# Kernel optimization log

Hardware: AMD Instinct MI355X
Metric: run time of the kernel (lower is better)

The kernel has to match this reference:

```python
import jax, jax.numpy as jnp
import numpy as np

D = 512; H = 8; DH = D // H; DFF = 4 * D; INNER = 2 * D; K = 31
B = 8; S = 1024
EPS = 1e-5


def layer_norm(x, g, b):
    m = jnp.mean(x, axis=-1, keepdims=True)
    v = jnp.mean(jnp.square(x - m), axis=-1, keepdims=True)
    return (x - m) * jax.lax.rsqrt(v + EPS) * g + b


def setup_inputs() -> dict:
    key = jax.random.key(0)
    ks = iter(jax.random.split(key, 32))
    w = lambda *s: jax.random.normal(next(ks), s, dtype=jnp.float32) * 0.02
    d = {
        "x": jax.random.normal(next(ks), (B, S, D), dtype=jnp.float32),
        # FF module 1
        "ln1_g": jnp.ones((D,)), "ln1_b": jnp.zeros((D,)),
        "ff1_w1": w(DFF, D), "ff1_b1": jnp.zeros((DFF,)),
        "ff1_w2": w(D, DFF), "ff1_b2": jnp.zeros((D,)),
        # attention
        "lna_g": jnp.ones((D,)), "lna_b": jnp.zeros((D,)),
        "qkv_w": w(3 * D, D), "qkv_b": jnp.zeros((3 * D,)),
        "out_w": w(D, D), "out_b": jnp.zeros((D,)),
        # conv module
        "lnc_g": jnp.ones((D,)), "lnc_b": jnp.zeros((D,)),
        "pw1_w": w(INNER, D), "pw1_b": jnp.zeros((INNER,)),
        "dw_w": w(D, 1, K), "dw_b": jnp.zeros((D,)),
        "bn_g": jnp.ones((D,)), "bn_b": jnp.zeros((D,)),
        "bn_mean": jnp.zeros((D,)), "bn_var": jnp.ones((D,)),
        "pw2_w": w(D, D), "pw2_b": jnp.zeros((D,)),
        # FF module 2
        "ln2_g": jnp.ones((D,)), "ln2_b": jnp.zeros((D,)),
        "ff2_w1": w(DFF, D), "ff2_b1": jnp.zeros((DFF,)),
        "ff2_w2": w(D, DFF), "ff2_b2": jnp.zeros((D,)),
        # final layer norm
        "lnf_g": jnp.ones((D,)), "lnf_b": jnp.zeros((D,)),
    }
    return d


def _ff(x, g, b, w1, b1, w2, b2):
    h = layer_norm(x, g, b)
    h = jax.nn.silu(h @ w1.T + b1)
    h = h @ w2.T + b2
    return h + x  # FeedForwardModule adds its own residual


def _attn(x, g, b, qkv_w, qkv_b, out_w, out_b):
    h = layer_norm(x, g, b)
    qkv = (h @ qkv_w.T + qkv_b).reshape(B, S, 3, H, DH)
    q, k, v = qkv[:, :, 0], qkv[:, :, 1], qkv[:, :, 2]  # [B,S,H,DH]
    scores = jnp.einsum('bqhd,bkhd->bhqk', q, k) / np.sqrt(DH).astype(np.float32)
    probs = jax.nn.softmax(scores, axis=-1)
    ctx = jnp.einsum('bhqk,bkhd->bqhd', probs, v).reshape(B, S, D)
    return ctx @ out_w.T + out_b


def _conv(x, g, b, pw1_w, pw1_b, dw_w, dw_b, bn_g, bn_b, bn_mean, bn_var, pw2_w, pw2_b):
    h = layer_norm(x, g, b)
    y = h @ pw1_w.T + pw1_b                      # [B,S,2D] pointwise conv1
    a, gate = jnp.split(y, 2, axis=-1)           # GLU along channel dim
    y = a * jax.nn.sigmoid(gate)                 # [B,S,D]
    y = y.transpose(0, 2, 1)                     # [B,D,S]
    y = jax.lax.conv_general_dilated(
        y, dw_w, window_strides=(1,), padding=((K // 2, K // 2),),
        dimension_numbers=('NCH', 'OIH', 'NCH'), feature_group_count=D)
    y = y + dw_b[None, :, None]
    y = (y - bn_mean[None, :, None]) * jax.lax.rsqrt(bn_var + EPS)[None, :, None]
    y = y * bn_g[None, :, None] + bn_b[None, :, None]
    y = jax.nn.silu(y)
    y = y.transpose(0, 2, 1)                     # [B,S,D]
    y = y @ pw2_w.T + pw2_b
    return y + x  # ConvModule adds its own residual


def reference(x, ln1_g, ln1_b, ff1_w1, ff1_b1, ff1_w2, ff1_b2,
              lna_g, lna_b, qkv_w, qkv_b, out_w, out_b,
              lnc_g, lnc_b, pw1_w, pw1_b, dw_w, dw_b,
              bn_g, bn_b, bn_mean, bn_var, pw2_w, pw2_b,
              ln2_g, ln2_b, ff2_w1, ff2_b1, ff2_w2, ff2_b2,
              lnf_g, lnf_b):
    x = x + 0.5 * _ff(x, ln1_g, ln1_b, ff1_w1, ff1_b1, ff1_w2, ff1_b2)
    x = x + _attn(x, lna_g, lna_b, qkv_w, qkv_b, out_w, out_b)
    x = x + _conv(x, lnc_g, lnc_b, pw1_w, pw1_b, dw_w, dw_b,
                  bn_g, bn_b, bn_mean, bn_var, pw2_w, pw2_b)
    x = x + 0.5 * _ff(x, ln2_g, ln2_b, ff2_w1, ff2_b1, ff2_w2, ff2_b2)
    return layer_norm(x, lnf_g, lnf_b)
```

## Files before the change

### kernel.cpp

```cpp
#include <hip/hip_runtime.h>
#include <hip/hip_bf16.h>

typedef __attribute__((ext_vector_type(8))) short bf16x8;
typedef __attribute__((ext_vector_type(4))) short bf16x4;
typedef __attribute__((ext_vector_type(4))) float f32x4;

#define NTOK 8192
#define SEQ  1024
#define NH   8

__device__ __forceinline__ float bfs2f(short s) {
  union { unsigned u; float f; } x; x.u = ((unsigned)(unsigned short)s) << 16; return x.f;
}
__device__ __forceinline__ short f2bfs(float f) {
  __hip_bfloat16 h = __float2bfloat16(f);
  return *reinterpret_cast<short*>(&h);
}
__device__ __forceinline__ float bfp2f(const __hip_bfloat16* p) {
  return bfs2f(*reinterpret_cast<const short*>(p));
}

__device__ __forceinline__ void gld16(const void* g, void* l) {
  __builtin_amdgcn_global_load_lds(
      (__attribute__((address_space(1))) void*)const_cast<void*>(g),
      (__attribute__((address_space(3))) void*)l, 16, 0, 0);
}

struct WSeg { const float* src; unsigned dst_off; unsigned nvec; };
struct WPack { WSeg s[8]; };

__global__ __launch_bounds__(256) void cast_wall_kernel(WPack p,
                                                        __hip_bfloat16* __restrict__ dst) {
  unsigned v = blockIdx.x * 256 + threadIdx.x;
#pragma unroll
  for (int t = 0; t < 8; ++t) {
    if (v < p.s[t].nvec) {
      const float* s = p.s[t].src + (size_t)v * 8;
      f32x4 a = *reinterpret_cast<const f32x4*>(s);
      f32x4 b = *reinterpret_cast<const f32x4*>(s + 4);
      bf16x8 o;
#pragma unroll
      for (int j = 0; j < 4; ++j) { o[j] = f2bfs(a[j]); o[4 + j] = f2bfs(b[j]); }
      *reinterpret_cast<bf16x8*>(reinterpret_cast<short*>(dst) +
                                 (size_t)(p.s[t].dst_off + v) * 8) = o;
      return;
    }
    v -= p.s[t].nvec;
  }
}

__global__ __launch_bounds__(256) void cast_dww_kernel(const float* __restrict__ src,
                                                       __hip_bfloat16* __restrict__ dst) {
  for (int k = 0; k < 31; ++k)
    for (int c = threadIdx.x; c < 512; c += 256)
      dst[k * 512 + c] = __float2bfloat16(src[c * 31 + k]);
}

struct PtrPack { const void* p[23]; };

__global__ __launch_bounds__(256) void cast_small_kernel(PtrPack pk,
                                                         __hip_bfloat16* __restrict__ dst) {
  constexpr int sizes[23] = {512, 512, 2048, 512, 512, 512, 1536, 512, 512, 512, 1024, 512,
                             512, 512, 512, 512, 512, 512, 512, 2048, 512, 512, 512};
  int off = 0;
  for (int t = 0; t < 23; ++t) {
    const int n = sizes[t];
    for (int i = threadIdx.x; i < n; i += 256)
      dst[off + i] = __float2bfloat16(((const float*)pk.p[t])[i]);
    off += n;
  }
}

__global__ void ws_bad_kernel(float* __restrict__ out) {
  if (threadIdx.x == 0) out[0] = 5000.f;
}

__global__ __launch_bounds__(256) void lnb_kernel(const __hip_bfloat16* __restrict__ in,
                                                  const __hip_bfloat16* __restrict__ g,
                                                  const __hip_bfloat16* __restrict__ b,
                                                  __hip_bfloat16* __restrict__ out) {
  const int wv = threadIdx.x >> 6, ln = threadIdx.x & 63;
  const int row = blockIdx.x * 4 + wv;
  bf16x8 iv = *reinterpret_cast<const bf16x8*>(in + (size_t)row * 512 + ln * 8);
  float v[8];
#pragma unroll
  for (int j = 0; j < 8; ++j) v[j] = bfs2f(iv[j]);
  float s = 0.f;
#pragma unroll
  for (int j = 0; j < 8; ++j) s += v[j];
  for (int m = 1; m < 64; m <<= 1) s += __shfl_xor(s, m);
  const float mean = s * (1.f / 512.f);
  float q = 0.f;
#pragma unroll
  for (int j = 0; j < 8; ++j) { float d = v[j] - mean; q += d * d; }
  for (int m = 1; m < 64; m <<= 1) q += __shfl_xor(q, m);
  const float rstd = rsqrtf(q * (1.f / 512.f) + 1e-5f);
  bf16x8 gg = *reinterpret_cast<const bf16x8*>(g + ln * 8);
  bf16x8 bb = *reinterpret_cast<const bf16x8*>(b + ln * 8);
  bf16x8 ov;
#pragma unroll
  for (int j = 0; j < 8; ++j)
    ov[j] = f2bfs((v[j] - mean) * rstd * bfs2f(gg[j]) + bfs2f(bb[j]));
  *reinterpret_cast<bf16x8*>(out + (size_t)row * 512 + ln * 8) = ov;
}

__global__ __launch_bounds__(256) void ln_kernel(const float* __restrict__ in,
                                                 const __hip_bfloat16* __restrict__ g,
                                                 const __hip_bfloat16* __restrict__ b,
                                                 __hip_bfloat16* __restrict__ out) {
  const int wv = threadIdx.x >> 6, ln = threadIdx.x & 63;
  const int row = blockIdx.x * 4 + wv;
  const float* p = in + (size_t)row * 512 + ln * 8;
  float v[8];
  {
    const f32x4* p4 = reinterpret_cast<const f32x4*>(p);
    f32x4 a = p4[0], c = p4[1];
#pragma unroll
    for (int j = 0; j < 4; ++j) { v[j] = a[j]; v[4 + j] = c[j]; }
  }
  float s = 0.f;
#pragma unroll
  for (int j = 0; j < 8; ++j) s += v[j];
  for (int m = 1; m < 64; m <<= 1) s += __shfl_xor(s, m);
  const float mean = s * (1.f / 512.f);
  float q = 0.f;
#pragma unroll
  for (int j = 0; j < 8; ++j) { float d = v[j] - mean; q += d * d; }
  for (int m = 1; m < 64; m <<= 1) q += __shfl_xor(q, m);
  const float rstd = rsqrtf(q * (1.f / 512.f) + 1e-5f);
  bf16x8 gg = *reinterpret_cast<const bf16x8*>(g + ln * 8);
  bf16x8 bb = *reinterpret_cast<const bf16x8*>(b + ln * 8);
  bf16x8 ov;
#pragma unroll
  for (int j = 0; j < 8; ++j)
    ov[j] = f2bfs((v[j] - mean) * rstd * bfs2f(gg[j]) + bfs2f(bb[j]));
  *reinterpret_cast<bf16x8*>(out + (size_t)row * 512 + ln * 8) = ov;
}

__global__ __launch_bounds__(256) void lnf_kernel(const __hip_bfloat16* __restrict__ in,
                                                  const __hip_bfloat16* __restrict__ g,
                                                  const __hip_bfloat16* __restrict__ b,
                                                  float* __restrict__ out) {
  const int wv = threadIdx.x >> 6, ln = threadIdx.x & 63;
  const int row = blockIdx.x * 4 + wv;
  bf16x8 iv = *reinterpret_cast<const bf16x8*>(in + (size_t)row * 512 + ln * 8);
  float v[8];
#pragma unroll
  for (int j = 0; j < 8; ++j) v[j] = bfs2f(iv[j]);
  float s = 0.f;
#pragma unroll
  for (int j = 0; j < 8; ++j) s += v[j];
  for (int m = 1; m < 64; m <<= 1) s += __shfl_xor(s, m);
  const float mean = s * (1.f / 512.f);
  float q = 0.f;
#pragma unroll
  for (int j = 0; j < 8; ++j) { float d = v[j] - mean; q += d * d; }
  for (int m = 1; m < 64; m <<= 1) q += __shfl_xor(q, m);
  const float rstd = rsqrtf(q * (1.f / 512.f) + 1e-5f);
  bf16x8 gg = *reinterpret_cast<const bf16x8*>(g + ln * 8);
  bf16x8 bb = *reinterpret_cast<const bf16x8*>(b + ln * 8);
  f32x4 o0, o1;
#pragma unroll
  for (int j = 0; j < 4; ++j) {
    o0[j] = (v[j] - mean) * rstd * bfs2f(gg[j]) + bfs2f(bb[j]);
    o1[j] = (v[4 + j] - mean) * rstd * bfs2f(gg[4 + j]) + bfs2f(bb[4 + j]);
  }
  float* op = out + (size_t)row * 512 + ln * 8;
  *reinterpret_cast<f32x4*>(op) = o0;
  *reinterpret_cast<f32x4*>(op + 4) = o1;
}

template <int EPI>
__global__ __launch_bounds__(256, 3) void gemm_bt(const __hip_bfloat16* __restrict__ A,
                                                  const __hip_bfloat16* __restrict__ W,
                                                  const __hip_bfloat16* __restrict__ bias,
                                                  __hip_bfloat16* __restrict__ outb,
                                                  __hip_bfloat16* __restrict__ vTout,
                                                  int K, int M) {
  __shared__ __align__(16) __hip_bfloat16 As[128 * 64];
  __shared__ __align__(16) __hip_bfloat16 Bs[128 * 64];
  const int tid = threadIdx.x;
  const int wv = tid >> 6, ln = tid & 63;
  const int hi = ln >> 4, lo = ln & 15;
  const int lo7 = lo & 7;
  const int gx = gridDim.x;
  const int nwg = gx * gridDim.y;
  const int t = blockIdx.y * gx + blockIdx.x;
  const int w = (t & 7) * (nwg >> 3) + (t >> 3);
  const int n0 = (w & (gx - 1)) * 128;
  const int m0 = (w / gx) * 128;
  const int wr = wv >> 1, wc = wv & 1;
  const int srow = ln >> 3;
  const int scolz = (((ln & 7) ^ srow) << 3);

  f32x4 acc[4][4] = {};

  for (int k0 = 0; k0 < K; k0 += 64) {
    __syncthreads();
#pragma unroll
    for (int i = 0; i < 4; ++i) {
      const int grp = i * 4 + wv;
      const int row = grp * 8 + srow;
      gld16(A + (size_t)(n0 + row) * K + k0 + scolz, As + grp * 512);
      gld16(W + (size_t)(m0 + row) * K + k0 + scolz, Bs + grp * 512);
    }
    __syncthreads();
#pragma unroll
    for (int kk2 = 0; kk2 < 2; ++kk2) {
      const int g0 = ((kk2 * 4 + hi) ^ lo7) << 3;
      bf16x8 af[4], bfr[4];
#pragma unroll
      for (int r = 0; r < 4; ++r)
        af[r] = *reinterpret_cast<const bf16x8*>(As + (wr * 64 + r * 16 + lo) * 64 + g0);
#pragma unroll
      for (int c = 0; c < 4; ++c)
        bfr[c] = *reinterpret_cast<const bf16x8*>(Bs + (wc * 64 + c * 16 + lo) * 64 + g0);
#pragma unroll
      for (int r = 0; r < 4; ++r)
#pragma unroll
        for (int c = 0; c < 4; ++c)
          acc[r][c] = __builtin_amdgcn_mfma_f32_16x16x32_bf16(af[r], bfr[c], acc[r][c], 0, 0, 0);
    }
  }

#pragma unroll
  for (int r = 0; r < 4; ++r) {
#pragma unroll
    for (int c = 0; c < 4; ++c) {
      const int m = m0 + wc * 64 + c * 16 + lo;
      const float bv = bfp2f(bias + m);
      const int nb = n0 + wr * 64 + r * 16 + hi * 4;
      if constexpr (EPI == 3) {
        if (m >= 1024) {
          const int hd = m - 1024;
          __hip_bfloat16* vp = vTout +
              ((size_t)((nb >> 10) * NH + (hd >> 6)) * 64 + (hd & 63)) * 1024 + (nb & 1023);
          bf16x4 vv;
#pragma unroll
          for (int j = 0; j < 4; ++j) vv[j] = f2bfs(acc[r][c][j] + bv);
          *reinterpret_cast<bf16x4*>(vp) = vv;
          continue;
        }
      }
#pragma unroll
      for (int j = 0; j < 4; ++j) {
        const int n = nb + j;
        float v = acc[r][c][j] + bv;
        if constexpr (EPI == 1) v = v / (1.f + __expf(-v));
        outb[(size_t)n * M + m] = __float2bfloat16(v);
      }
    }
  }
}

template <int RF32>
__global__ __launch_bounds__(256, 4) void gemm64_resid(const __hip_bfloat16* __restrict__ A,
                                                       const __hip_bfloat16* __restrict__ W,
                                                       const __hip_bfloat16* __restrict__ bias,
                                                       const void* __restrict__ rsrc,
                                                       __hip_bfloat16* __restrict__ resid,
                                                       int K, float alpha, float beta) {
  __shared__ __align__(16) __hip_bfloat16 As[64 * 64];
  __shared__ __align__(16) __hip_bfloat16 Bs[128 * 64];
  const int tid = threadIdx.x;
  const int wv = tid >> 6, ln = tid & 63;
  const int hi = ln >> 4, lo = ln & 15;
  const int lo7 = lo & 7;
  const int gx = gridDim.x;
  const int nwg = gx * gridDim.y;
  const int t = blockIdx.y * gx + blockIdx.x;
  const int w = (t & 7) * (nwg >> 3) + (t >> 3);
  const int n0 = (w & (gx - 1)) * 64;
  const int m0 = (w / gx) * 128;
  const int wr = wv >> 1, wc = wv & 1;
  const int srow = ln >> 3;
  const int scolz = (((ln & 7) ^ srow) << 3);

  f32x4 acc[2][4] = {};

  for (int k0 = 0; k0 < K; k0 += 64) {
    __syncthreads();
#pragma unroll
    for (int i = 0; i < 2; ++i) {
      const int grp = i * 4 + wv;
      gld16(A + (size_t)(n0 + grp * 8 + srow) * K + k0 + scolz, As + grp * 512);
    }
#pragma unroll
    for (int i = 0; i < 4; ++i) {
      const int grp = i * 4 + wv;
      gld16(W + (size_t)(m0 + grp * 8 + srow) * K + k0 + scolz, Bs + grp * 512);
    }
    __syncthreads();
#pragma unroll
    for (int kk2 = 0; kk2 < 2; ++kk2) {
      const int g0 = ((kk2 * 4 + hi) ^ lo7) << 3;
      bf16x8 af[2], bfr[4];
#pragma unroll
      for (int r = 0; r < 2; ++r)
        af[r] = *reinterpret_cast<const bf16x8*>(As + (wr * 32 + r * 16 + lo) * 64 + g0);
#pragma unroll
      for (int c = 0; c < 4; ++c)
        bfr[c] = *reinterpret_cast<const bf16x8*>(Bs + (wc * 64 + c * 16 + lo) * 64 + g0);
#pragma unroll
      for (int r = 0; r < 2; ++r)
#pragma unroll
        for (int c = 0; c < 4; ++c)
          acc[r][c] = __builtin_amdgcn_mfma_f32_16x16x32_bf16(af[r], bfr[c], acc[r][c], 0, 0, 0);
    }
  }

#pragma unroll
  for (int r = 0; r < 2; ++r) {
#pragma unroll
    for (int c = 0; c < 4; ++c) {
      const int m = m0 + wc * 64 + c * 16 + lo;
      const float bv = bfp2f(bias + m);
#pragma unroll
      for (int j = 0; j < 4; ++j) {
        const int n = n0 + wr * 32 + r * 16 + hi * 4 + j;
        const size_t idx = (size_t)n * 512 + m;
        const float rv = RF32 ? ((const float*)rsrc)[idx]
                              : bfs2f(((const short*)rsrc)[idx]);
        resid[idx] = __float2bfloat16(alpha * rv + beta * (acc[r][c][j] + bv));
      }
    }
  }
}

__global__ __launch_bounds__(256, 3) void gemm_glu(const __hip_bfloat16* __restrict__ A,
                                                   const __hip_bfloat16* __restrict__ W,
                                                   const __hip_bfloat16* __restrict__ bias,
                                                   __hip_bfloat16* __restrict__ outb,
                                                   int K) {
  __shared__ __align__(16) __hip_bfloat16 As[64 * 64];
  __shared__ __align__(16) __hip_bfloat16 Ba[128 * 64];
  __shared__ __align__(16) __hip_bfloat16 Bg[128 * 64];
  const int tid = threadIdx.x;
  const int wv = tid >> 6, ln = tid & 63;
  const int hi = ln >> 4, lo = ln & 15;
  const int lo7 = lo & 7;
  const int gx = gridDim.x;
  const int nwg = gx * gridDim.y;
  const int t = blockIdx.y * gx + blockIdx.x;
  const int w = (t & 7) * (nwg >> 3) + (t >> 3);
  const int n0 = (w & (gx - 1)) * 64;
  const int m0 = (w / gx) * 128;
  const int wr = wv >> 1, wc = wv & 1;
  const int srow = ln >> 3;
  const int scolz = (((ln & 7) ^ srow) << 3);

  f32x4 acca[2][4] = {}, accg[2][4] = {};

  for (int k0 = 0; k0 < K; k0 += 64) {
    __syncthreads();
#pragma unroll
    for (int i = 0; i < 2; ++i) {
      const int grp = i * 4 + wv;
      gld16(A + (size_t)(n0 + grp * 8 + srow) * K + k0 + scolz, As + grp * 512);
    }
#pragma unroll
    for (int i = 0; i < 4; ++i) {
      const int grp = i * 4 + wv;
      gld16(W + (size_t)(m0 + grp * 8 + srow) * K + k0 + scolz, Ba + grp * 512);
      gld16(W + (size_t)(512 + m0 + grp * 8 + srow) * K + k0 + scolz, Bg + grp * 512);
    }
    __syncthreads();
#pragma unroll
    for (int kk2 = 0; kk2 < 2; ++kk2) {
      const int g0 = ((kk2 * 4 + hi) ^ lo7) << 3;
      bf16x8 af[2], ba[4], bg[4];
#pragma unroll
      for (int r = 0; r < 2; ++r)
        af[r] = *reinterpret_cast<const bf16x8*>(As + (wr * 32 + r * 16 + lo) * 64 + g0);
#pragma unroll
      for (int c = 0; c < 4; ++c) {
        ba[c] = *reinterpret_cast<const bf16x8*>(Ba + (wc * 64 + c * 16 + lo) * 64 + g0);
        bg[c] = *reinterpret_cast<const bf16x8*>(Bg + (wc * 64 + c * 16 + lo) * 64 + g0);
      }
#pragma unroll
      for (int r = 0; r < 2; ++r)
#pragma unroll
        for (int c = 0; c < 4; ++c) {
          acca[r][c] = __builtin_amdgcn_mfma_f32_16x16x32_bf16(af[r], ba[c], acca[r][c], 0, 0, 0);
          accg[r][c] = __builtin_amdgcn_mfma_f32_16x16x32_bf16(af[r], bg[c], accg[r][c], 0, 0, 0);
        }
    }
  }

#pragma unroll
  for (int r = 0; r < 2; ++r) {
#pragma unroll
    for (int c = 0; c < 4; ++c) {
      const int m = m0 + wc * 64 + c * 16 + lo;
      const float bva = bfp2f(bias + m);
      const float bvg = bfp2f(bias + 512 + m);
#pragma unroll
      for (int j = 0; j < 4; ++j) {
        const int n = n0 + wr * 32 + r * 16 + hi * 4 + j;
        const float a = acca[r][c][j] + bva;
        const float g = accg[r][c][j] + bvg;
        outb[(size_t)n * 512 + m] = __float2bfloat16(a / (1.f + __expf(-g)));
      }
    }
  }
}

__global__ __launch_bounds__(256, 3) void attn_kernel(const __hip_bfloat16* __restrict__ qkv,
                                                      const __hip_bfloat16* __restrict__ vT,
                                                      __hip_bfloat16* __restrict__ ctx) {
  __shared__ __align__(16) short Ks[2][64 * 64];
  __shared__ __align__(16) short Vs[2][64 * 64];
  __shared__ __align__(16) short P[4][16][64];
  const int tid = threadIdx.x;
  const int wv = tid >> 6, ln = tid & 63;
  const int hi = ln >> 4, lo = ln & 15;
  const int lo7 = lo & 7;
  const int blk = ((blockIdx.x & 7) << 6) | (blockIdx.x >> 3);
  const int qt = blk & 7, h = (blk >> 3) & 7, b = blk >> 6;
  const int q0 = qt * 128 + wv * 16;

  const int srow8 = ln >> 3;
  const int gsrc = (ln & 7) ^ srow8;

  bf16x8 aq0a, aq1a, aq0b, aq1b;
  {
    const __hip_bfloat16* qpa = qkv + (size_t)(b * SEQ + q0 + lo) * 1536 + h * 64 + hi * 8;
    const __hip_bfloat16* qpb = qpa + (size_t)64 * 1536;
    bf16x8 r0 = *reinterpret_cast<const bf16x8*>(qpa);
    bf16x8 r1 = *reinterpret_cast<const bf16x8*>(qpa + 32);
    bf16x8 r2 = *reinterpret_cast<const bf16x8*>(qpb);
    bf16x8 r3 = *reinterpret_cast<const bf16x8*>(qpb + 32);
#pragma unroll
    for (int j = 0; j < 8; ++j) {
      aq0a[j] = f2bfs(bfs2f(r0[j]) * 0.125f);
      aq1a[j] = f2bfs(bfs2f(r1[j]) * 0.125f);
      aq0b[j] = f2bfs(bfs2f(r2[j]) * 0.125f);
      aq1b[j] = f2bfs(bfs2f(r3[j]) * 0.125f);
    }
  }

  const __hip_bfloat16* kbase = qkv + 512 + h * 64 + (size_t)b * SEQ * 1536;
  const __hip_bfloat16* vbase = vT + (size_t)(b * NH + h) * 64 * 1024;

  f32x4 oaccA[4] = {}, oaccB[4] = {};
  float lrowA[4] = {0.f, 0.f, 0.f, 0.f};
  float lrowB[4] = {0.f, 0.f, 0.f, 0.f};

#pragma unroll
  for (int c = 0; c < 2; ++c) {
    const int r = c * 32 + wv * 8 + srow8;
    gld16(kbase + (size_t)r * 1536 + gsrc * 8, &Ks[0][(c * 32 + wv * 8) * 64]);
    gld16(vbase + (size_t)r * 1024 + gsrc * 8, &Vs[0][(c * 32 + wv * 8) * 64]);
  }
  __syncthreads();

  int cb = 0;
  for (int kt = 0; kt < 16; ++kt) {
    if (kt < 15) {
      const int kb2 = (kt + 1) * 64;
#pragma unroll
      for (int c = 0; c < 2; ++c) {
        const int r = c * 32 + wv * 8 + srow8;
        gld16(kbase + (size_t)(kb2 + r) * 1536 + gsrc * 8,
              &Ks[cb ^ 1][(c * 32 + wv * 8) * 64]);
        gld16(vbase + (size_t)r * 1024 + kb2 + gsrc * 8,
              &Vs[cb ^ 1][(c * 32 + wv * 8) * 64]);
      }
    }

    bf16x8 bk0[4], bk1[4];
#pragma unroll
    for (int nt = 0; nt < 4; ++nt) {
      const short* kr = &Ks[cb][(nt * 16 + lo) * 64];
      bk0[nt] = *reinterpret_cast<const bf16x8*>(kr + ((hi ^ lo7) << 3));
      bk1[nt] = *reinterpret_cast<const bf16x8*>(kr + (((hi + 4) ^ lo7) << 3));
    }
    f32x4 scA[4] = {}, scB[4] = {};
#pragma unroll
    for (int nt = 0; nt < 4; ++nt) {
      scA[nt] = __builtin_amdgcn_mfma_f32_16x16x32_bf16(aq0a, bk0[nt], scA[nt], 0, 0, 0);
      scA[nt] = __builtin_amdgcn_mfma_f32_16x16x32_bf16(aq1a, bk1[nt], scA[nt], 0, 0, 0);
      scB[nt] = __builtin_amdgcn_mfma_f32_16x16x32_bf16(aq0b, bk0[nt], scB[nt], 0, 0, 0);
      scB[nt] = __builtin_amdgcn_mfma_f32_16x16x32_bf16(aq1b, bk1[nt], scB[nt], 0, 0, 0);
    }

    bf16x8 bv0[4], bv1[4];
#pragma unroll
    for (int dt = 0; dt < 4; ++dt) {
      const short* vr = &Vs[cb][(dt * 16 + lo) * 64];
      bv0[dt] = *reinterpret_cast<const bf16x8*>(vr + ((hi ^ lo7) << 3));
      bv1[dt] = *reinterpret_cast<const bf16x8*>(vr + (((hi + 4) ^ lo7) << 3));
    }

#pragma unroll
    for (int j = 0; j < 4; ++j) {
      const int prow = hi * 4 + j;
      const int pswz = (prow & 7) << 3;
#pragma unroll
      for (int nt = 0; nt < 4; ++nt) {
        const float p = __expf(scA[nt][j]);
        P[wv][prow][(nt * 16 + lo) ^ pswz] = f2bfs(p);
        lrowA[j] += p;
      }
    }
    asm volatile("" ::: "memory");
    {
      const short* pr = &P[wv][lo][0];
      bf16x8 ap0 = *reinterpret_cast<const bf16x8*>(pr + ((hi ^ lo7) << 3));
      bf16x8 ap1 = *reinterpret_cast<const bf16x8*>(pr + (((hi + 4) ^ lo7) << 3));
#pragma unroll
      for (int dt = 0; dt < 4; ++dt) {
        oaccA[dt] = __builtin_amdgcn_mfma_f32_16x16x32_bf16(ap0, bv0[dt], oaccA[dt], 0, 0, 0);
        oaccA[dt] = __builtin_amdgcn_mfma_f32_16x16x32_bf16(ap1, bv1[dt], oaccA[dt], 0, 0, 0);
      }
    }
    asm volatile("" ::: "memory");

#pragma unroll
    for (int j = 0; j < 4; ++j) {
      const int prow = hi * 4 + j;
      const int pswz = (prow & 7) << 3;
#pragma unroll
      for (int nt = 0; nt < 4; ++nt) {
        const float p = __expf(scB[nt][j]);
        P[wv][prow][(nt * 16 + lo) ^ pswz] = f2bfs(p);
        lrowB[j] += p;
      }
    }
    asm volatile("" ::: "memory");
    {
      const short* pr = &P[wv][lo][0];
      bf16x8 ap0 = *reinterpret_cast<const bf16x8*>(pr + ((hi ^ lo7) << 3));
      bf16x8 ap1 = *reinterpret_cast<const bf16x8*>(pr + (((hi + 4) ^ lo7) << 3));
#pragma unroll
      for (int dt = 0; dt < 4; ++dt) {
        oaccB[dt] = __builtin_amdgcn_mfma_f32_16x16x32_bf16(ap0, bv0[dt], oaccB[dt], 0, 0, 0);
        oaccB[dt] = __builtin_amdgcn_mfma_f32_16x16x32_bf16(ap1, bv1[dt], oaccB[dt], 0, 0, 0);
      }
    }
    __syncthreads();
    cb ^= 1;
  }

#pragma unroll
  for (int j = 0; j < 4; ++j) {
    float sa = lrowA[j], sb = lrowB[j];
    sa += __shfl_xor(sa, 1); sb += __shfl_xor(sb, 1);
    sa += __shfl_xor(sa, 2); sb += __shfl_xor(sb, 2);
    sa += __shfl_xor(sa, 4); sb += __shfl_xor(sb, 4);
    sa += __shfl_xor(sa, 8); sb += __shfl_xor(sb, 8);
    lrowA[j] = sa; lrowB[j] = sb;
  }

#pragma unroll
  for (int dt = 0; dt < 4; ++dt)
#pragma unroll
    for (int j = 0; j < 4; ++j) {
      const int d = h * 64 + dt * 16 + lo;
      const int na = b * SEQ + q0 + hi * 4 + j;
      ctx[(size_t)na * 512 + d] = __float2bfloat16(oaccA[dt][j] / lrowA[j]);
      const int nb = na + 64;
      ctx[(size_t)nb * 512 + d] = __float2bfloat16(oaccB[dt][j] / lrowB[j]);
    }
}

__global__ __launch_bounds__(256) void dwconv8_kernel(const __hip_bfloat16* __restrict__ cin,
                                                      const __hip_bfloat16* __restrict__ wkT,
                                                      const __hip_bfloat16* __restrict__ cb,
                                                      const __hip_bfloat16* __restrict__ bng,
                                                      const __hip_bfloat16* __restrict__ bnb,
                                                      const __hip_bfloat16* __restrict__ bnm,
                                                      const __hip_bfloat16* __restrict__ bnv,
                                                      __hip_bfloat16* __restrict__ outp) {
  const int i = blockIdx.x * 256 + threadIdx.x;
  const int c8 = i & 63;
  const int n = i >> 6;
  const int t = n & 1023;
  const int base = n - t;
  const int co = c8 * 8;

  float acc[8];
  {
    bf16x8 bv = *reinterpret_cast<const bf16x8*>(cb + co);
#pragma unroll
    for (int j = 0; j < 8; ++j) acc[j] = bfs2f(bv[j]);
  }
  const int k0 = (t >= 15) ? 0 : (15 - t);
  const int k1 = (t <= SEQ - 16) ? 31 : (SEQ - 1 - t + 16);
  const short* cin_s = reinterpret_cast<const short*>(cin);
  const short* wk_s = reinterpret_cast<const short*>(wkT);
  for (int k = k0; k < k1; ++k) {
    const int ts = t + k - 15;
    bf16x8 xv = *reinterpret_cast<const bf16x8*>(cin_s + (((size_t)(base + ts)) << 9) + co);
    bf16x8 wv = *reinterpret_cast<const bf16x8*>(wk_s + k * 512 + co);
#pragma unroll
    for (int j = 0; j < 8; ++j) acc[j] += bfs2f(xv[j]) * bfs2f(wv[j]);
  }
  bf16x8 g = *reinterpret_cast<const bf16x8*>(bng + co);
  bf16x8 bb = *reinterpret_cast<const bf16x8*>(bnb + co);
  bf16x8 bm = *reinterpret_cast<const bf16x8*>(bnm + co);
  bf16x8 bvv = *reinterpret_cast<const bf16x8*>(bnv + co);
  bf16x8 ov;
#pragma unroll
  for (int j = 0; j < 8; ++j) {
    const float scl = bfs2f(g[j]) * rsqrtf(bfs2f(bvv[j]) + 1e-5f);
    float v = (acc[j] - bfs2f(bm[j])) * scl + bfs2f(bb[j]);
    v = v / (1.f + __expf(-v));
    ov[j] = f2bfs(v);
  }
  *reinterpret_cast<bf16x8*>(reinterpret_cast<short*>(outp) + ((size_t)n << 9) + co) = ov;
}

extern "C" void kernel_launch(void* const* d_in, const int* in_sizes, int n_in,
                              void* d_out, int out_size, void* d_ws, size_t ws_size,
                              hipStream_t stream) {
  float* out = (float*)d_out;
  if (ws_size < ((size_t)80 << 20)) {
    ws_bad_kernel<<<1, 64, 0, stream>>>(out);
    return;
  }

  const float* x = (const float*)d_in[0];

  char* ws = (char*)d_ws;
  __hip_bfloat16* xsb = (__hip_bfloat16*)ws;
  __hip_bfloat16* t0 = (__hip_bfloat16*)(ws + ((size_t)16 << 20));
  __hip_bfloat16* t1 = (__hip_bfloat16*)(ws + ((size_t)24 << 20));
  __hip_bfloat16* t2 = (__hip_bfloat16*)(ws + ((size_t)56 << 20));
  __hip_bfloat16* wc = (__hip_bfloat16*)(ws + ((size_t)64 << 20));
  __hip_bfloat16* vT = t1 + (size_t)NTOK * 1536;

  __hip_bfloat16* wc_ff1_w1 = wc + 0;
  __hip_bfloat16* wc_ff1_w2 = wc + 1048576;
  __hip_bfloat16* wc_qkv_w  = wc + 2097152;
  __hip_bfloat16* wc_out_w  = wc + 2883584;
  __hip_bfloat16* wc_pw1_w  = wc + 3145728;
  __hip_bfloat16* wc_pw2_w  = wc + 3670016;
  __hip_bfloat16* wc_ff2_w1 = wc + 3932160;
  __hip_bfloat16* wc_ff2_w2 = wc + 4980736;
  __hip_bfloat16* wc_dwT    = wc + 6029312;
  __hip_bfloat16* sm        = wc + 6045184;
  __hip_bfloat16* c_ln1_g = sm + 0,     *c_ln1_b = sm + 512,   *c_ff1_b1 = sm + 1024;
  __hip_bfloat16* c_ff1_b2 = sm + 3072, *c_lna_g = sm + 3584,  *c_lna_b = sm + 4096;
  __hip_bfloat16* c_qkv_b = sm + 4608,  *c_out_b = sm + 6144,  *c_lnc_g = sm + 6656;
  __hip_bfloat16* c_lnc_b = sm + 7168,  *c_pw1_b = sm + 7680,  *c_dw_b = sm + 8704;
  __hip_bfloat16* c_bn_g = sm + 9216,   *c_bn_b = sm + 9728,   *c_bn_m = sm + 10240;
  __hip_bfloat16* c_bn_v = sm + 10752,  *c_pw2_b = sm + 11264, *c_ln2_g = sm + 11776;
  __hip_bfloat16* c_ln2_b = sm + 12288, *c_ff2_b1 = sm + 12800, *c_ff2_b2 = sm + 14848;
  __hip_bfloat16* c_lnf_g = sm + 15360, *c_lnf_b = sm + 15872;

  {
    WPack wp;
    wp.s[0] = {(const float*)d_in[3],  0,      131072};
    wp.s[1] = {(const float*)d_in[5],  131072, 131072};
    wp.s[2] = {(const float*)d_in[9],  262144, 98304};
    wp.s[3] = {(const float*)d_in[11], 360448, 32768};
    wp.s[4] = {(const float*)d_in[15], 393216, 65536};
    wp.s[5] = {(const float*)d_in[23], 458752, 32768};
    wp.s[6] = {(const float*)d_in[27], 491520, 131072};
    wp.s[7] = {(const float*)d_in[29], 622592, 131072};
    cast_wall_kernel<<<2944, 256, 0, stream>>>(wp, wc);
  }
  cast_dww_kernel<<<1, 256, 0, stream>>>((const float*)d_in[17], wc_dwT);
  PtrPack pk;
  const int small_idx[23] = {1, 2, 4, 6, 7, 8, 10, 12, 13, 14, 16, 18,
                             19, 20, 21, 22, 24, 25, 26, 28, 30, 31, 32};
  for (int t = 0; t < 23; ++t) pk.p[t] = d_in[small_idx[t]];
  cast_small_kernel<<<1, 256, 0, stream>>>(pk, sm);

  ln_kernel<<<2048, 256, 0, stream>>>(x, c_ln1_g, c_ln1_b, t0);
  gemm_bt<1><<<dim3(64, 16), 256, 0, stream>>>(t0, wc_ff1_w1, c_ff1_b1, t1, nullptr, 512, 2048);
  gemm64_resid<1><<<dim3(128, 4), 256, 0, stream>>>(t1, wc_ff1_w2, c_ff1_b2, x, xsb, 2048, 1.5f, 0.5f);

  lnb_kernel<<<2048, 256, 0, stream>>>(xsb, c_lna_g, c_lna_b, t0);
  gemm_bt<3><<<dim3(64, 12), 256, 0, stream>>>(t0, wc_qkv_w, c_qkv_b, t1, vT, 512, 1536);
  attn_kernel<<<512, 256, 0, stream>>>(t1, vT, t2);
  gemm64_resid<0><<<dim3(128, 4), 256, 0, stream>>>(t2, wc_out_w, c_out_b, xsb, xsb, 512, 1.0f, 1.0f);

  lnb_kernel<<<2048, 256, 0, stream>>>(xsb, c_lnc_g, c_lnc_b, t0);
  gemm_glu<<<dim3(128, 4), 256, 0, stream>>>(t0, wc_pw1_w, c_pw1_b, t2, 512);
  dwconv8_kernel<<<2048, 256, 0, stream>>>(t2, wc_dwT, c_dw_b, c_bn_g, c_bn_b, c_bn_m, c_bn_v, t0);
  gemm64_resid<0><<<dim3(128, 4), 256, 0, stream>>>(t0, wc_pw2_w, c_pw2_b, xsb, xsb, 512, 2.0f, 1.0f);

  lnb_kernel<<<2048, 256, 0, stream>>>(xsb, c_ln2_g, c_ln2_b, t0);
  gemm_bt<1><<<dim3(64, 16), 256, 0, stream>>>(t0, wc_ff2_w1, c_ff2_b1, t1, nullptr, 512, 2048);
  gemm64_resid<0><<<dim3(128, 4), 256, 0, stream>>>(t1, wc_ff2_w2, c_ff2_b2, xsb, xsb, 2048, 1.5f, 0.5f);

  lnf_kernel<<<2048, 256, 0, stream>>>(xsb, c_lnf_g, c_lnf_b, out);
}
```

Baseline: 287.7 us.

## Tile depthwise conv through LDS with halo rows and swizzled layout

The depthwise conv kernel now stages a 64-token by 64-channel tile plus a 15-row halo on each side, along with the filter weights, into shared memory using an XOR swizzle. Each thread then computes 16 channels for one token from LDS. Previously each thread re-read 31 input rows from global memory or cache. This removes redundant global loads at the cost of an LDS stage, a block barrier, and halo overhead (94 rows loaded per 64 tokens).

```diff
diff --git a/kernel.cpp b/kernel.cpp
--- a/kernel.cpp
+++ b/kernel.cpp
@@ -564,51 +564,85 @@
     }
 }
 
-__global__ __launch_bounds__(256) void dwconv8_kernel(const __hip_bfloat16* __restrict__ cin,
-                                                      const __hip_bfloat16* __restrict__ wkT,
-                                                      const __hip_bfloat16* __restrict__ cb,
-                                                      const __hip_bfloat16* __restrict__ bng,
-                                                      const __hip_bfloat16* __restrict__ bnb,
-                                                      const __hip_bfloat16* __restrict__ bnm,
-                                                      const __hip_bfloat16* __restrict__ bnv,
-                                                      __hip_bfloat16* __restrict__ outp) {
-  const int i = blockIdx.x * 256 + threadIdx.x;
-  const int c8 = i & 63;
-  const int n = i >> 6;
-  const int t = n & 1023;
-  const int base = n - t;
-  const int co = c8 * 8;
-
-  float acc[8];
+__global__ __launch_bounds__(256, 4) void dwconv_lds_kernel(
+    const __hip_bfloat16* __restrict__ cin, const __hip_bfloat16* __restrict__ wkT,
+    const __hip_bfloat16* __restrict__ cb, const __hip_bfloat16* __restrict__ bng,
+    const __hip_bfloat16* __restrict__ bnb, const __hip_bfloat16* __restrict__ bnm,
+    const __hip_bfloat16* __restrict__ bnv, __hip_bfloat16* __restrict__ outp) {
+  __shared__ __align__(16) short Ls[94][64];
+  __shared__ __align__(16) short Wsh[31][64];
+  const int tid = threadIdx.x;
+  const int tok0 = blockIdx.x * 64;
+  const int ch0 = blockIdx.y * 64;
+  const int s0 = tok0 & ~1023;
+
+  for (int idx = tid; idx < 94 * 8; idx += 256) {
+    const int r = idx >> 3, gsl = idx & 7;
+    const int gr = tok0 - 15 + r;
+    bf16x8 v;
+    if (gr >= s0 && gr < s0 + 1024) {
+      v = *reinterpret_cast<const bf16x8*>(
+          reinterpret_cast<const short*>(cin) + (size_t)gr * 512 + ch0 + gsl * 8);
+    } else {
+#pragma unroll
+      for (int j = 0; j < 8; ++j) v[j] = 0;
+    }
+    *reinterpret_cast<bf16x8*>(&Ls[r][(gsl ^ (r & 7)) * 8]) = v;
+  }
+  for (int idx = tid; idx < 31 * 8; idx += 256) {
+    const int k = idx >> 3, gsl = idx & 7;
+    *reinterpret_cast<bf16x8*>(&Wsh[k][(gsl ^ (k & 7)) * 8]) =
+        *reinterpret_cast<const bf16x8*>(
+            reinterpret_cast<const short*>(wkT) + k * 512 + ch0 + gsl * 8);
+  }
+  __syncthreads();
+
+  const int tl = tid >> 2;
+  const int cg = (tid & 3) * 2;
+  float acc[16];
   {
-    bf16x8 bv = *reinterpret_cast<const bf16x8*>(cb + co);
-#pragma unroll
-    for (int j = 0; j < 8; ++j) acc[j] = bfs2f(bv[j]);
-  }
-  const int k0 = (t >= 15) ? 0 : (15 - t);
-  const int k1 = (t <= SEQ - 16) ? 31 : (SEQ - 1 - t + 16);
-  const short* cin_s = reinterpret_cast<const short*>(cin);
-  const short* wk_s = reinterpret_cast<const short*>(wkT);
-  for (int k = k0; k < k1; ++k) {
-    const int ts = t + k - 15;
-    bf16x8 xv = *reinterpret_cast<const bf16x8*>(cin_s + (((size_t)(base + ts)) << 9) + co);
-    bf16x8 wv = *reinterpret_cast<const bf16x8*>(wk_s + k * 512 + co);
-#pragma unroll
-    for (int j = 0; j < 8; ++j) acc[j] += bfs2f(xv[j]) * bfs2f(wv[j]);
-  }
-  bf16x8 g = *reinterpret_cast<const bf16x8*>(bng + co);
-  bf16x8 bb = *reinterpret_cast<const bf16x8*>(bnb + co);
-  bf16x8 bm = *reinterpret_cast<const bf16x8*>(bnm + co);
-  bf16x8 bvv = *reinterpret_cast<const bf16x8*>(bnv + co);
-  bf16x8 ov;
+    bf16x8 b0 = *reinterpret_cast<const bf16x8*>(cb + ch0 + cg * 8);
+    bf16x8 b1 = *reinterpret_cast<const bf16x8*>(cb + ch0 + cg * 8 + 8);
+#pragma unroll
+    for (int j = 0; j < 8; ++j) { acc[j] = bfs2f(b0[j]); acc[8 + j] = bfs2f(b1[j]); }
+  }
+  for (int k = 0; k < 31; ++k) {
+    const int lr = tl + k;
+    bf16x8 x0 = *reinterpret_cast<const bf16x8*>(&Ls[lr][(cg ^ (lr & 7)) * 8]);
+    bf16x8 x1 = *reinterpret_cast<const bf16x8*>(&Ls[lr][((cg + 1) ^ (lr & 7)) * 8]);
+    bf16x8 w0 = *reinterpret_cast<const bf16x8*>(&Wsh[k][(cg ^ (k & 7)) * 8]);
+    bf16x8 w1 = *reinterpret_cast<const bf16x8*>(&Wsh[k][((cg + 1) ^ (k & 7)) * 8]);
+#pragma unroll
+    for (int j = 0; j < 8; ++j) {
+      acc[j] += bfs2f(x0[j]) * bfs2f(w0[j]);
+      acc[8 + j] += bfs2f(x1[j]) * bfs2f(w1[j]);
+    }
+  }
+  const int n = tok0 + tl;
+  const int co = ch0 + cg * 8;
+  bf16x8 g0 = *reinterpret_cast<const bf16x8*>(bng + co);
+  bf16x8 g1 = *reinterpret_cast<const bf16x8*>(bng + co + 8);
+  bf16x8 bb0 = *reinterpret_cast<const bf16x8*>(bnb + co);
+  bf16x8 bb1 = *reinterpret_cast<const bf16x8*>(bnb + co + 8);
+  bf16x8 bm0 = *reinterpret_cast<const bf16x8*>(bnm + co);
+  bf16x8 bm1 = *reinterpret_cast<const bf16x8*>(bnm + co + 8);
+  bf16x8 bv0 = *reinterpret_cast<const bf16x8*>(bnv + co);
+  bf16x8 bv1 = *reinterpret_cast<const bf16x8*>(bnv + co + 8);
+  bf16x8 o0, o1;
 #pragma unroll
   for (int j = 0; j < 8; ++j) {
-    const float scl = bfs2f(g[j]) * rsqrtf(bfs2f(bvv[j]) + 1e-5f);
-    float v = (acc[j] - bfs2f(bm[j])) * scl + bfs2f(bb[j]);
-    v = v / (1.f + __expf(-v));
-    ov[j] = f2bfs(v);
-  }
-  *reinterpret_cast<bf16x8*>(reinterpret_cast<short*>(outp) + ((size_t)n << 9) + co) = ov;
+    float s0f = bfs2f(g0[j]) * rsqrtf(bfs2f(bv0[j]) + 1e-5f);
+    float v0 = (acc[j] - bfs2f(bm0[j])) * s0f + bfs2f(bb0[j]);
+    v0 = v0 / (1.f + __expf(-v0));
+    o0[j] = f2bfs(v0);
+    float s1f = bfs2f(g1[j]) * rsqrtf(bfs2f(bv1[j]) + 1e-5f);
+    float v1 = (acc[8 + j] - bfs2f(bm1[j])) * s1f + bfs2f(bb1[j]);
+    v1 = v1 / (1.f + __expf(-v1));
+    o1[j] = f2bfs(v1);
+  }
+  short* op = reinterpret_cast<short*>(outp) + (size_t)n * 512 + co;
+  *reinterpret_cast<bf16x8*>(op) = o0;
+  *reinterpret_cast<bf16x8*>(op + 8) = o1;
 }
 
 extern "C" void kernel_launch(void* const* d_in, const int* in_sizes, int n_in,
@@ -679,7 +713,7 @@
 
   lnb_kernel<<<2048, 256, 0, stream>>>(xsb, c_lnc_g, c_lnc_b, t0);
   gemm_glu<<<dim3(128, 4), 256, 0, stream>>>(t0, wc_pw1_w, c_pw1_b, t2, 512);
-  dwconv8_kernel<<<2048, 256, 0, stream>>>(t2, wc_dwT, c_dw_b, c_bn_g, c_bn_b, c_bn_m, c_bn_v, t0);
+  dwconv_lds_kernel<<<dim3(128, 8), 256, 0, stream>>>(t2, wc_dwT, c_dw_b, c_bn_g, c_bn_b, c_bn_m, c_bn_v, t0);
   gemm64_resid<0><<<dim3(128, 4), 256, 0, stream>>>(t0, wc_pw2_w, c_pw2_b, xsb, xsb, 512, 2.0f, 1.0f);
 
   lnb_kernel<<<2048, 256, 0, stream>>>(xsb, c_ln2_g, c_ln2_b, t0);
```

New measurement: 291.7 us. Within noise of the previous version (+1.4%).
